# Optimization experiments

Measured on AMD Instinct MI355X. Metric: run time of the kernel, lower is better.

The kernel has to match this reference:

```python
import jax, jax.numpy as jnp
import numpy as np

D_MODEL = 1024
N_HEADS = 16
D_K = D_MODEL // N_HEADS
NEG = -1e9


def setup_inputs() -> dict:
    key = jax.random.key(0)
    ks = jax.random.split(key, 14)
    b, sq, sk = 4, 2048, 2048
    s = 1.0 / np.sqrt(D_MODEL)
    inp = {
        "Q": jax.random.normal(ks[0], (b, sq, D_MODEL), jnp.float32),
        "K": jax.random.normal(ks[1], (b, sk, D_MODEL), jnp.float32),
        "V": jax.random.normal(ks[2], (b, sk, D_MODEL), jnp.float32),
        "mask": jax.random.randint(ks[3], (b, sk), 0, 2, jnp.int32),
        "relative_logits": jax.random.normal(ks[4], (1, N_HEADS, sq, sk), jnp.float32),
        "Wq": jax.random.normal(ks[5], (D_MODEL, D_MODEL), jnp.float32) * s,
        "bq": jnp.zeros((D_MODEL,), jnp.float32),
        "Wk": jax.random.normal(ks[6], (D_MODEL, D_MODEL), jnp.float32) * s,
        "bk": jnp.zeros((D_MODEL,), jnp.float32),
        "Wv": jax.random.normal(ks[7], (D_MODEL, D_MODEL), jnp.float32) * s,
        "bv": jnp.zeros((D_MODEL,), jnp.float32),
        "Wo": jax.random.normal(ks[8], (D_MODEL, D_MODEL), jnp.float32) * s,
        "bo": jnp.zeros((D_MODEL,), jnp.float32),
    }
    return inp


def reference(Q, K, V, mask, relative_logits, Wq, bq, Wk, bk, Wv, bv, Wo, bo):
    b, sq, _ = Q.shape
    sk = K.shape[1]
    # projections -> [b, h, s, d_k]
    q = (Q @ Wq + bq).reshape(b, sq, N_HEADS, D_K).transpose(0, 2, 1, 3)
    k = (K @ Wk + bk).reshape(b, sk, N_HEADS, D_K).transpose(0, 2, 1, 3)
    v = (V @ Wv + bv).reshape(b, sk, N_HEADS, D_K).transpose(0, 2, 1, 3)
    scores = jnp.einsum("bhqd,bhkd->bhqk", q, k) / jnp.sqrt(jnp.float32(D_K))
    scores = scores + relative_logits
    # 2D mask [b, sk] -> [b, 1, 1, sk]; masked_fill where mask == 0
    m = mask[:, None, None, :]
    scores = jnp.where(m == 0, jnp.float32(NEG), scores)
    attn = jax.nn.softmax(scores, axis=-1)  # dropout = identity (eval mode)
    out = jnp.einsum("bhqk,bhkd->bhqd", attn, v)
    out = out.transpose(0, 2, 1, 3).reshape(b, sq, N_HEADS * D_K)
    out = out @ Wo + bo
    return (out, attn)
```

## Files before the change

### kernel.cpp

```cpp
#include <hip/hip_runtime.h>
#include <hip/hip_fp16.h>

typedef _Float16 f16;
typedef __attribute__((ext_vector_type(4))) _Float16 f16x4;
typedef __attribute__((ext_vector_type(8))) _Float16 f16x8;
typedef __attribute__((ext_vector_type(4))) float f32x4;

#define S_LEN 2048
#define D_MODEL 1024
#define N_HEADS 16
#define D_K 64
#define BATCH 4

#define EXP_NEG8 3.35462627903e-4f

#define LBAR() do { asm volatile("s_waitcnt lgkmcnt(0)" ::: "memory"); \
                    __builtin_amdgcn_s_barrier(); } while (0)

__global__ void cvt_f32_f16(const float* __restrict__ src, f16* __restrict__ dst, int n4) {
  int i = blockIdx.x * blockDim.x + threadIdx.x;
  if (i < n4) {
    const float4 v = reinterpret_cast<const float4*>(src)[i];
    f16x4 h;
    h.x = (f16)v.x; h.y = (f16)v.y; h.z = (f16)v.z; h.w = (f16)v.w;
    reinterpret_cast<f16x4*>(dst)[i] = h;
  }
}

__global__ void cvt3(const float* __restrict__ s0, const float* __restrict__ s1,
                     const float* __restrict__ s2, f16* __restrict__ d0, f16* __restrict__ d1,
                     f16* __restrict__ d2, int n4) {
  const float* s = blockIdx.y == 0 ? s0 : (blockIdx.y == 1 ? s1 : s2);
  f16* d = blockIdx.y == 0 ? d0 : (blockIdx.y == 1 ? d1 : d2);
  int i = blockIdx.x * blockDim.x + threadIdx.x;
  if (i < n4) {
    const float4 v = reinterpret_cast<const float4*>(s)[i];
    f16x4 h;
    h.x = (f16)v.x; h.y = (f16)v.y; h.z = (f16)v.z; h.w = (f16)v.w;
    reinterpret_cast<f16x4*>(d)[i] = h;
  }
}

__global__ void wtrans4(const float* __restrict__ W0, const float* __restrict__ W1,
                        const float* __restrict__ W2, const float* __restrict__ W3,
                        f16* __restrict__ T0, f16* __restrict__ T1, f16* __restrict__ T2,
                        f16* __restrict__ T3) {
  const float* W = blockIdx.z == 0 ? W0 : (blockIdx.z == 1 ? W1 : (blockIdx.z == 2 ? W2 : W3));
  f16* WT = blockIdx.z == 0 ? T0 : (blockIdx.z == 1 ? T1 : (blockIdx.z == 2 ? T2 : T3));
  __shared__ float tile[32][33];
  const int n0 = blockIdx.x * 32, k0 = blockIdx.y * 32;
  const int tx = threadIdx.x, ty = threadIdx.y;
#pragma unroll
  for (int i = 0; i < 4; ++i)
    tile[ty + i * 8][tx] = W[(size_t)(k0 + ty + i * 8) * D_MODEL + n0 + tx];
  __syncthreads();
#pragma unroll
  for (int i = 0; i < 4; ++i)
    WT[(size_t)(n0 + ty + i * 8) * D_MODEL + k0 + tx] = (f16)tile[tx][ty + i * 8];
}

__global__ __launch_bounds__(256, 3) void gemmQKV(const f16* __restrict__ Qh, const f16* __restrict__ Kh,
                                                  const f16* __restrict__ Vh, const f16* __restrict__ WqT,
                                                  const f16* __restrict__ WkT, const f16* __restrict__ WvT,
                                                  const float* __restrict__ bq, const float* __restrict__ bk,
                                                  const float* __restrict__ bv, f16* __restrict__ qb,
                                                  f16* __restrict__ kb, f16* __restrict__ vTb) {
  const int z = blockIdx.z;
  const f16* A = z == 0 ? Qh : (z == 1 ? Kh : Vh);
  const f16* BT = z == 0 ? WqT : (z == 1 ? WkT : WvT);
  const float* bias = z == 0 ? bq : (z == 1 ? bk : bv);

  __shared__ f16 As[2][128 * 40];
  __shared__ f16 Bs[2][128 * 40];
  const int t = threadIdx.x;
  const int lane = t & 63, wid = t >> 6;
  const int wm = wid >> 1, wn = wid & 1;
  const int lr = lane & 15, lg = lane >> 4;
  const int bm = blockIdx.y * 128, bn = blockIdx.x * 128;

  f32x4 acc[4][4] = {};

  const int r0s = t >> 2, g0 = (t & 3) * 8;
  const f16* gA0 = &A[(size_t)(bm + r0s) * 1024 + g0];
  const f16* gA1 = gA0 + (size_t)64 * 1024;
  const f16* gB0 = &BT[(size_t)(bn + r0s) * 1024 + g0];
  const f16* gB1 = gB0 + (size_t)64 * 1024;
  const int dst0 = r0s * 40 + g0, dst1 = (r0s + 64) * 40 + g0;

  int4 sA0, sA1, sB0, sB1;
  auto GLOAD = [&](int k0) {
    sA0 = *reinterpret_cast<const int4*>(gA0 + k0);
    sA1 = *reinterpret_cast<const int4*>(gA1 + k0);
    sB0 = *reinterpret_cast<const int4*>(gB0 + k0);
    sB1 = *reinterpret_cast<const int4*>(gB1 + k0);
  };
  auto DSW = [&](int bb) {
    *reinterpret_cast<int4*>(&As[bb][dst0]) = sA0;
    *reinterpret_cast<int4*>(&As[bb][dst1]) = sA1;
    *reinterpret_cast<int4*>(&Bs[bb][dst0]) = sB0;
    *reinterpret_cast<int4*>(&Bs[bb][dst1]) = sB1;
  };
  auto LDF = [&](int bb, int kk, f16x4 (&af)[4], f16x4 (&bf)[4]) {
#pragma unroll
    for (int mf = 0; mf < 4; ++mf)
      af[mf] = *reinterpret_cast<const f16x4*>(&As[bb][(wm * 64 + mf * 16 + lr) * 40 + kk * 16 + 4 * lg]);
#pragma unroll
    for (int nf = 0; nf < 4; ++nf)
      bf[nf] = *reinterpret_cast<const f16x4*>(&Bs[bb][(wn * 64 + nf * 16 + lr) * 40 + kk * 16 + 4 * lg]);
  };

  GLOAD(0);
  DSW(0);
  LBAR();
  if (z != 2) {
#pragma unroll 1
    for (int k = 0; k < 32; ++k) {
      if (k + 1 < 32) GLOAD((k + 1) * 32);
#pragma unroll
      for (int kk = 0; kk < 2; ++kk) {
        f16x4 af[4], bf[4];
        LDF(k & 1, kk, af, bf);
#pragma unroll
        for (int mf = 0; mf < 4; ++mf)
#pragma unroll
          for (int nf = 0; nf < 4; ++nf)
            acc[mf][nf] = __builtin_amdgcn_mfma_f32_16x16x16f16(af[mf], bf[nf], acc[mf][nf], 0, 0, 0);
      }
      if (k + 1 < 32) {
        DSW((k + 1) & 1);
        LBAR();
      }
    }
  } else {
#pragma unroll 1
    for (int k = 0; k < 32; ++k) {
      if (k + 1 < 32) GLOAD((k + 1) * 32);
#pragma unroll
      for (int kk = 0; kk < 2; ++kk) {
        f16x4 af[4], bf[4];
        LDF(k & 1, kk, af, bf);
#pragma unroll
        for (int mf = 0; mf < 4; ++mf)
#pragma unroll
          for (int nf = 0; nf < 4; ++nf)
            acc[mf][nf] = __builtin_amdgcn_mfma_f32_16x16x16f16(bf[nf], af[mf], acc[mf][nf], 0, 0, 0);
      }
      if (k + 1 < 32) {
        DSW((k + 1) & 1);
        LBAR();
      }
    }
  }

  if (z != 2) {
    const float scale = z == 0 ? 0.125f : 1.f;
    f16* outp = z == 0 ? qb : kb;
#pragma unroll
    for (int mf = 0; mf < 4; ++mf)
#pragma unroll
      for (int nf = 0; nf < 4; ++nf)
#pragma unroll
        for (int i = 0; i < 4; ++i) {
          const int mrow = bm + wm * 64 + mf * 16 + 4 * lg + i;
          const int ncol = bn + wn * 64 + nf * 16 + lr;
          const float v = (acc[mf][nf][i] + bias[ncol]) * scale;
          const int b = mrow >> 11, s = mrow & 2047;
          const int h = ncol >> 6, d = ncol & 63;
          outp[((size_t)(b * N_HEADS + h) * S_LEN + s) * D_K + d] = (f16)v;
        }
  } else {
#pragma unroll
    for (int mf = 0; mf < 4; ++mf)
#pragma unroll
      for (int nf = 0; nf < 4; ++nf)
#pragma unroll
        for (int i = 0; i < 4; ++i) {
          const int srow = bm + wm * 64 + mf * 16 + lr;
          const int dcol = bn + wn * 64 + nf * 16 + 4 * lg + i;
          const float v = acc[mf][nf][i] + bias[dcol];
          const int b = srow >> 11, s = srow & 2047;
          const int h = dcol >> 6, d = dcol & 63;
          vTb[((size_t)(b * N_HEADS + h) * D_K + d) * S_LEN + s] = (f16)v;
        }
  }
}

__global__ __launch_bounds__(256, 3) void gemmO(const f16* __restrict__ A, const f16* __restrict__ BT,
                                                const float* __restrict__ bias, float* __restrict__ outp) {
  __shared__ f16 As[2][128 * 40];
  __shared__ f16 Bs[2][128 * 40];
  const int t = threadIdx.x;
  const int lane = t & 63, wid = t >> 6;
  const int wm = wid >> 1, wn = wid & 1;
  const int lr = lane & 15, lg = lane >> 4;
  const int bm = blockIdx.y * 128, bn = blockIdx.x * 128;

  f32x4 acc[4][4] = {};

  const int r0s = t >> 2, g0 = (t & 3) * 8;
  const f16* gA0 = &A[(size_t)(bm + r0s) * 1024 + g0];
  const f16* gA1 = gA0 + (size_t)64 * 1024;
  const f16* gB0 = &BT[(size_t)(bn + r0s) * 1024 + g0];
  const f16* gB1 = gB0 + (size_t)64 * 1024;
  const int dst0 = r0s * 40 + g0, dst1 = (r0s + 64) * 40 + g0;

  int4 sA0, sA1, sB0, sB1;
  auto GLOAD = [&](int k0) {
    sA0 = *reinterpret_cast<const int4*>(gA0 + k0);
    sA1 = *reinterpret_cast<const int4*>(gA1 + k0);
    sB0 = *reinterpret_cast<const int4*>(gB0 + k0);
    sB1 = *reinterpret_cast<const int4*>(gB1 + k0);
  };
  auto DSW = [&](int bb) {
    *reinterpret_cast<int4*>(&As[bb][dst0]) = sA0;
    *reinterpret_cast<int4*>(&As[bb][dst1]) = sA1;
    *reinterpret_cast<int4*>(&Bs[bb][dst0]) = sB0;
    *reinterpret_cast<int4*>(&Bs[bb][dst1]) = sB1;
  };

  GLOAD(0);
  DSW(0);
  LBAR();
#pragma unroll 1
  for (int k = 0; k < 32; ++k) {
    if (k + 1 < 32) GLOAD((k + 1) * 32);
#pragma unroll
    for (int kk = 0; kk < 2; ++kk) {
      f16x4 af[4], bf[4];
#pragma unroll
      for (int mf = 0; mf < 4; ++mf)
        af[mf] = *reinterpret_cast<const f16x4*>(&As[k & 1][(wm * 64 + mf * 16 + lr) * 40 + kk * 16 + 4 * lg]);
#pragma unroll
      for (int nf = 0; nf < 4; ++nf)
        bf[nf] = *reinterpret_cast<const f16x4*>(&Bs[k & 1][(wn * 64 + nf * 16 + lr) * 40 + kk * 16 + 4 * lg]);
#pragma unroll
      for (int mf = 0; mf < 4; ++mf)
#pragma unroll
        for (int nf = 0; nf < 4; ++nf)
          acc[mf][nf] = __builtin_amdgcn_mfma_f32_16x16x16f16(af[mf], bf[nf], acc[mf][nf], 0, 0, 0);
    }
    if (k + 1 < 32) {
      DSW((k + 1) & 1);
      LBAR();
    }
  }

#pragma unroll
  for (int mf = 0; mf < 4; ++mf)
#pragma unroll
    for (int nf = 0; nf < 4; ++nf)
#pragma unroll
      for (int i = 0; i < 4; ++i) {
        const int mrow = bm + wm * 64 + mf * 16 + 4 * lg + i;
        const int ncol = bn + wn * 64 + nf * 16 + lr;
        outp[(size_t)mrow * D_MODEL + ncol] = acc[mf][nf][i] + bias[ncol];
      }
}

__global__ __launch_bounds__(256, 3) void attn_fused2(const f16* __restrict__ qg, const f16* __restrict__ kg,
                                                      const f16* __restrict__ vTg, const f16* __restrict__ rel16,
                                                      const int* __restrict__ mask, float* __restrict__ attn_out,
                                                      f16* __restrict__ ctx) {
  const int b = blockIdx.x & 3, qt = blockIdx.x >> 2;
  const int h = blockIdx.y;
  const int t = threadIdx.x, w = t >> 6, lane = t & 63;
  const int lr = lane & 15, lg = lane >> 4;
  const int lr7 = lr & 7;
  const int Ld8 = lane >> 3, Lm8 = lane & 7;

  __shared__ f16 Kc[2][64 * 64];
  __shared__ f16 Vc[2][64 * 64];
  __shared__ f16 Rc[2][64 * 64];
  __shared__ f16 maskh[S_LEN];

  for (int i = t; i < S_LEN; i += 256) maskh[i] = mask[b * S_LEN + i] ? (f16)EXP_NEG8 : (f16)0.f;

  const size_t bh = (size_t)(b * N_HEADS + h);
  const f16* qbh = qg + bh * S_LEN * D_K;
  const f16* kbh = kg + bh * S_LEN * D_K;
  const f16* vbh = vTg + bh * (size_t)D_K * S_LEN;
  const f16* relh = rel16 + (size_t)h * S_LEN * S_LEN;

  const int r0 = qt * 64 + w * 16;
  const int myq = r0 + lr;
  float* attnq = attn_out + bh * (size_t)S_LEN * S_LEN + (size_t)myq * S_LEN;

  const int row0 = w * 16 + Ld8;
  const int row1 = row0 + 8;
  const f16* gK0 = kbh + (size_t)row0 * D_K + Lm8 * 8;
  const f16* gK1 = kbh + (size_t)row1 * D_K + Lm8 * 8;
  const f16* gV0 = vbh + (size_t)row0 * S_LEN + Lm8 * 8;
  const f16* gV1 = vbh + (size_t)row1 * S_LEN + Lm8 * 8;
  const f16* gR0 = relh + (size_t)(qt * 64 + row0) * S_LEN + Lm8 * 8;
  const f16* gR1 = relh + (size_t)(qt * 64 + row1) * S_LEN + Lm8 * 8;
  const int dK0 = row0 * 64 + ((Lm8 ^ Ld8) << 3);
  const int dK1 = row1 * 64 + ((Lm8 ^ Ld8) << 3);
  const int dVR0 = row0 * 64 + ((((Lm8 << 1) ^ (Ld8 << 1)) & 15) << 2);
  const int dVR1 = row1 * 64 + ((((Lm8 << 1) ^ (Ld8 << 1)) & 15) << 2);

  f16x8 qf8[2];
#pragma unroll
  for (int p = 0; p < 2; ++p)
    qf8[p] = *reinterpret_cast<const f16x8*>(&qbh[(size_t)myq * D_K + 32 * p + 8 * lg]);

  int4 sK0, sK1, sV0, sV1, sR0, sR1;
  auto GK = [&](int c0) {
    sK0 = *reinterpret_cast<const int4*>(gK0 + (size_t)c0 * D_K);
    sK1 = *reinterpret_cast<const int4*>(gK1 + (size_t)c0 * D_K);
  };
  auto GV = [&](int c0) {
    sV0 = *reinterpret_cast<const int4*>(gV0 + c0);
    sV1 = *reinterpret_cast<const int4*>(gV1 + c0);
  };
  auto GR = [&](int c0) {
    sR0 = *reinterpret_cast<const int4*>(gR0 + c0);
    sR1 = *reinterpret_cast<const int4*>(gR1 + c0);
  };
  auto DSW1 = [&](int bb) {
    *reinterpret_cast<int4*>(&Kc[bb][dK0]) = sK0;
    *reinterpret_cast<int4*>(&Kc[bb][dK1]) = sK1;
    *reinterpret_cast<int4*>(&Rc[bb][dVR0]) = sR0;
    *reinterpret_cast<int4*>(&Rc[bb][dVR1]) = sR1;
  };
  auto DSW2 = [&](int bb) {
    *reinterpret_cast<int4*>(&Kc[bb][dK0]) = sK0;
    *reinterpret_cast<int4*>(&Kc[bb][dK1]) = sK1;
    *reinterpret_cast<int4*>(&Vc[bb][dVR0]) = sV0;
    *reinterpret_cast<int4*>(&Vc[bb][dVR1]) = sV1;
    *reinterpret_cast<int4*>(&Rc[bb][dVR0]) = sR0;
    *reinterpret_cast<int4*>(&Rc[bb][dVR1]) = sR1;
  };

  auto SCORES = [&](int bb, f32x4 (&sc)[4]) {
#pragma unroll
    for (int p = 0; p < 2; ++p) {
      const f16x4 qlo = __builtin_shufflevector(qf8[p], qf8[p], 0, 1, 2, 3);
      const f16x4 qhi = __builtin_shufflevector(qf8[p], qf8[p], 4, 5, 6, 7);
#pragma unroll
      for (int j = 0; j < 4; ++j) {
        const f16x8 kv = *reinterpret_cast<const f16x8*>(
            &Kc[bb][(16 * j + lr) * 64 + (((4 * p + lg) ^ lr7) << 3)]);
        sc[j] = __builtin_amdgcn_mfma_f32_16x16x16f16(
            __builtin_shufflevector(kv, kv, 0, 1, 2, 3), qlo, sc[j], 0, 0, 0);
        sc[j] = __builtin_amdgcn_mfma_f32_16x16x16f16(
            __builtin_shufflevector(kv, kv, 4, 5, 6, 7), qhi, sc[j], 0, 0, 0);
      }
    }
  };

  float sum = 0.f;
  GK(0);
  GR(0);
  DSW1(0);
  LBAR();
#pragma unroll 1
  for (int c = 0; c < 32; ++c) {
    if (c + 1 < 32) {
      GK((c + 1) * 64);
      GR((c + 1) * 64);
    }
    const int bb = c & 1;
    f32x4 sc[4] = {};
    SCORES(bb, sc);
#pragma unroll
    for (int j = 0; j < 4; ++j) {
      const int sgp = ((4 * j + lg) ^ (lr7 << 1)) & 15;
      const f16x4 rl = *reinterpret_cast<const f16x4*>(&Rc[bb][(w * 16 + lr) * 64 + (sgp << 2)]);
      const int col = c * 64 + 16 * j + 4 * lg;
      const f16x4 mh = *reinterpret_cast<const f16x4*>(&maskh[col]);
      sum += __expf(sc[j][0] + (float)rl[0]) * (float)mh[0] +
             __expf(sc[j][1] + (float)rl[1]) * (float)mh[1] +
             __expf(sc[j][2] + (float)rl[2]) * (float)mh[2] +
             __expf(sc[j][3] + (float)rl[3]) * (float)mh[3];
    }
    if (c + 1 < 32) {
      DSW1((c + 1) & 1);
      LBAR();
    }
  }
  sum += __shfl_xor(sum, 16, 64);
  sum += __shfl_xor(sum, 32, 64);
  const float inv = 1.f / sum;

  f32x4 pv[4] = {};
  GK(0);
  GV(0);
  GR(0);
  DSW2(0);
  LBAR();
#pragma unroll 1
  for (int c = 0; c < 32; ++c) {
    if (c + 1 < 32) {
      GK((c + 1) * 64);
      GV((c + 1) * 64);
      GR((c + 1) * 64);
    }
    const int bb = c & 1;
    f32x4 sc[4] = {};
    SCORES(bb, sc);
#pragma unroll
    for (int j = 0; j < 4; ++j) {
      const int sgp = ((4 * j + lg) ^ (lr7 << 1)) & 15;
      const f16x4 rl = *reinterpret_cast<const f16x4*>(&Rc[bb][(w * 16 + lr) * 64 + (sgp << 2)]);
      const int col = c * 64 + 16 * j + 4 * lg;
      const f16x4 mh = *reinterpret_cast<const f16x4*>(&maskh[col]);
      const float a0 = __expf(sc[j][0] + (float)rl[0]) * (float)mh[0] * inv;
      const float a1 = __expf(sc[j][1] + (float)rl[1]) * (float)mh[1] * inv;
      const float a2 = __expf(sc[j][2] + (float)rl[2]) * (float)mh[2] * inv;
      const float a3 = __expf(sc[j][3] + (float)rl[3]) * (float)mh[3] * inv;
      f32x4 av = {a0, a1, a2, a3};
      __builtin_nontemporal_store(av, reinterpret_cast<f32x4*>(&attnq[col]));
      f16x4 pf;
      pf.x = (f16)a0; pf.y = (f16)a1; pf.z = (f16)a2; pf.w = (f16)a3;
#pragma unroll
      for (int nf = 0; nf < 4; ++nf) {
        const f16x4 vf = *reinterpret_cast<const f16x4*>(&Vc[bb][(nf * 16 + lr) * 64 + (sgp << 2)]);
        pv[nf] = __builtin_amdgcn_mfma_f32_16x16x16f16(pf, vf, pv[nf], 0, 0, 0);
      }
    }
    if (c + 1 < 32) {
      DSW2((c + 1) & 1);
      LBAR();
    }
  }

#pragma unroll
  for (int nf = 0; nf < 4; ++nf)
#pragma unroll
    for (int i = 0; i < 4; ++i)
      ctx[(size_t)(b * S_LEN + r0 + 4 * lg + i) * D_MODEL + h * D_K + nf * 16 + lr] =
          (f16)pv[nf][i];
}

__global__ __launch_bounds__(256) void attn_single(const f16* __restrict__ qg, const f16* __restrict__ kg,
                                                   const f16* __restrict__ vTg, const float* __restrict__ relp,
                                                   const int* __restrict__ mask, float* __restrict__ attn_out,
                                                   f16* __restrict__ ctx) {
  const int b = blockIdx.x & 3, qt = blockIdx.x >> 2;
  const int h = blockIdx.y;
  const int t = threadIdx.x, w = t >> 6, lane = t & 63;
  const int lr = lane & 15, lg = lane >> 4;
  __shared__ float mask_f[S_LEN];

  for (int i = t; i < S_LEN; i += 256) mask_f[i] = mask[b * S_LEN + i] ? EXP_NEG8 : 0.f;
  __syncthreads();

  const size_t bh = (size_t)(b * N_HEADS + h);
  const f16* qbh = qg + bh * S_LEN * D_K;
  const f16* kbh = kg + bh * S_LEN * D_K;
  const f16* vbh = vTg + bh * (size_t)D_K * S_LEN;

  const int r0 = qt * 64 + w * 16;
  const int myq = r0 + lr;

  const float* relq32 = relp + (size_t)h * S_LEN * S_LEN + (size_t)myq * S_LEN;
  float* attnq = attn_out + bh * (size_t)S_LEN * S_LEN + (size_t)myq * S_LEN;

  f16x8 qf8[2];
#pragma unroll
  for (int p = 0; p < 2; ++p)
    qf8[p] = *reinterpret_cast<const f16x8*>(&qbh[(size_t)myq * D_K + 32 * p + 8 * lg]);

  float sum = 0.f;
  f32x4 pv[4] = {};

  auto CH = [&](int c0) {
    f32x4 sc[4] = {};
#pragma unroll
    for (int p = 0; p < 2; ++p) {
      const f16x4 qlo = __builtin_shufflevector(qf8[p], qf8[p], 0, 1, 2, 3);
      const f16x4 qhi = __builtin_shufflevector(qf8[p], qf8[p], 4, 5, 6, 7);
#pragma unroll
      for (int j = 0; j < 4; ++j) {
        const f16x8 kv = *reinterpret_cast<const f16x8*>(
            &kbh[(size_t)(c0 + 16 * j + lr) * D_K + 32 * p + 8 * lg]);
        sc[j] = __builtin_amdgcn_mfma_f32_16x16x16f16(
            __builtin_shufflevector(kv, kv, 0, 1, 2, 3), qlo, sc[j], 0, 0, 0);
        sc[j] = __builtin_amdgcn_mfma_f32_16x16x16f16(
            __builtin_shufflevector(kv, kv, 4, 5, 6, 7), qhi, sc[j], 0, 0, 0);
      }
    }
#pragma unroll
    for (int j = 0; j < 4; ++j) {
      const int col = c0 + 16 * j + 4 * lg;
      const float4 rl = *reinterpret_cast<const float4*>(&relq32[col]);
      const float4 mk = *reinterpret_cast<const float4*>(&mask_f[col]);
      const float a0 = __expf(sc[j][0] + rl.x) * mk.x;
      const float a1 = __expf(sc[j][1] + rl.y) * mk.y;
      const float a2 = __expf(sc[j][2] + rl.z) * mk.z;
      const float a3 = __expf(sc[j][3] + rl.w) * mk.w;
      sum += a0 + a1 + a2 + a3;
      f16x4 pf;
      pf.x = (f16)a0; pf.y = (f16)a1; pf.z = (f16)a2; pf.w = (f16)a3;
      *reinterpret_cast<float4*>(&attnq[col]) = make_float4(a0, a1, a2, a3);
#pragma unroll
      for (int nf = 0; nf < 4; ++nf) {
        const f16x4 vf = *reinterpret_cast<const f16x4*>(&vbh[(size_t)(nf * 16 + lr) * S_LEN + col]);
        pv[nf] = __builtin_amdgcn_mfma_f32_16x16x16f16(pf, vf, pv[nf], 0, 0, 0);
      }
    }
  };

#pragma unroll 1
  for (int c0 = 0; c0 < S_LEN; c0 += 64) CH(c0);

  sum += __shfl_xor(sum, 16, 64);
  sum += __shfl_xor(sum, 32, 64);
  const float inv = 1.f / sum;

  float ivr[4];
#pragma unroll
  for (int i = 0; i < 4; ++i) ivr[i] = __shfl(inv, 4 * lg + i, 64);
#pragma unroll
  for (int nf = 0; nf < 4; ++nf)
#pragma unroll
    for (int i = 0; i < 4; ++i)
      ctx[(size_t)(b * S_LEN + r0 + 4 * lg + i) * D_MODEL + h * D_K + nf * 16 + lr] =
          (f16)(pv[nf][i] * ivr[i]);

  float4* aw4 = reinterpret_cast<float4*>(attn_out + bh * (size_t)S_LEN * S_LEN + (size_t)r0 * S_LEN);
#pragma unroll 1
  for (int it = 0; it < 128; it += 4) {
#pragma unroll
    for (int u = 0; u < 4; ++u) {
      const float iv = __shfl(inv, (it + u) >> 3, 64);
      float4 v = aw4[(it + u) * 64 + lane];
      v.x *= iv; v.y *= iv; v.z *= iv; v.w *= iv;
      aw4[(it + u) * 64 + lane] = v;
    }
  }
}

extern "C" void kernel_launch(void* const* d_in, const int* in_sizes, int n_in,
                              void* d_out, int out_size, void* d_ws, size_t ws_size,
                              hipStream_t stream) {
  const float* Q    = (const float*)d_in[0];
  const float* K    = (const float*)d_in[1];
  const float* V    = (const float*)d_in[2];
  const int*   mask = (const int*)d_in[3];
  const float* rel  = (const float*)d_in[4];
  const float* Wq   = (const float*)d_in[5];
  const float* bq   = (const float*)d_in[6];
  const float* Wk   = (const float*)d_in[7];
  const float* bk   = (const float*)d_in[8];
  const float* Wv   = (const float*)d_in[9];
  const float* bv   = (const float*)d_in[10];
  const float* Wo   = (const float*)d_in[11];
  const float* bo   = (const float*)d_in[12];

  char* wsb = (char*)d_ws;
  const size_t XSZ = (size_t)BATCH * S_LEN * D_MODEL * sizeof(f16);
  const size_t WSZ = (size_t)D_MODEL * D_MODEL * sizeof(f16);
  f16* Qh  = (f16*)(wsb);
  f16* Kh  = (f16*)(wsb + XSZ);
  f16* Vh  = (f16*)(wsb + 2 * XSZ);
  f16* WqT = (f16*)(wsb + 3 * XSZ);
  f16* WkT = (f16*)(wsb + 3 * XSZ + WSZ);
  f16* WvT = (f16*)(wsb + 3 * XSZ + 2 * WSZ);
  f16* WoT = (f16*)(wsb + 3 * XSZ + 3 * WSZ);
  f16* qb  = (f16*)(wsb + 3 * XSZ + 4 * WSZ);
  f16* kb  = (f16*)(wsb + 4 * XSZ + 4 * WSZ);
  f16* vTb = (f16*)(wsb + 5 * XSZ + 4 * WSZ);
  f16* ctx = (f16*)(wsb + 6 * XSZ + 4 * WSZ);

  const size_t BASE  = 7 * XSZ + 4 * WSZ;
  const size_t RELSZ = (size_t)N_HEADS * S_LEN * S_LEN * sizeof(f16);
  f16* rel16 = (f16*)(wsb + BASE);
  const bool r16 = ws_size >= BASE + RELSZ;

  float* out0 = (float*)d_out;
  float* attn = out0 + (size_t)BATCH * S_LEN * D_MODEL;

  const int n4 = BATCH * S_LEN * D_MODEL / 4;
  cvt3<<<dim3(n4 / 256, 3), 256, 0, stream>>>(Q, K, V, Qh, Kh, Vh, n4);
  wtrans4<<<dim3(32, 32, 4), dim3(32, 8), 0, stream>>>(Wq, Wk, Wv, Wo, WqT, WkT, WvT, WoT);
  if (r16) {
    const int nr4 = N_HEADS * S_LEN * S_LEN / 4;
    cvt_f32_f16<<<dim3(nr4 / 256), 256, 0, stream>>>(rel, rel16, nr4);
  }

  gemmQKV<<<dim3(8, 64, 3), 256, 0, stream>>>(Qh, Kh, Vh, WqT, WkT, WvT, bq, bk, bv, qb, kb, vTb);

  if (r16) {
    attn_fused2<<<dim3(BATCH * (S_LEN / 64), N_HEADS), 256, 0, stream>>>(qb, kb, vTb, rel16, mask,
                                                                         attn, ctx);
  } else {
    attn_single<<<dim3(BATCH * (S_LEN / 64), N_HEADS), 256, 0, stream>>>(qb, kb, vTb, rel, mask,
                                                                         attn, ctx);
  }

  gemmO<<<dim3(8, 64), 256, 0, stream>>>(ctx, WoT, bo, out0);
}
```

Measured before the change: 694.1 us.

## Process two 64-row query tiles per block in fused attention kernel

Result: faster. 674.0 us (median of 2 runs) (-2.9%).

```diff
diff --git a/kernel.cpp b/kernel.cpp
--- a/kernel.cpp
+++ b/kernel.cpp
@@ -257,7 +257,7 @@
       }
 }
 
-__global__ __launch_bounds__(256, 3) void attn_fused2(const f16* __restrict__ qg, const f16* __restrict__ kg,
+__global__ __launch_bounds__(256, 2) void attn_fused2(const f16* __restrict__ qg, const f16* __restrict__ kg,
                                                       const f16* __restrict__ vTg, const f16* __restrict__ rel16,
                                                       const int* __restrict__ mask, float* __restrict__ attn_out,
                                                       f16* __restrict__ ctx) {
@@ -270,7 +270,7 @@
 
   __shared__ f16 Kc[2][64 * 64];
   __shared__ f16 Vc[2][64 * 64];
-  __shared__ f16 Rc[2][64 * 64];
+  __shared__ f16 Rc[2][128 * 64];
   __shared__ f16 maskh[S_LEN];
 
   for (int i = t; i < S_LEN; i += 256) maskh[i] = mask[b * S_LEN + i] ? (f16)EXP_NEG8 : (f16)0.f;
@@ -281,9 +281,10 @@
   const f16* vbh = vTg + bh * (size_t)D_K * S_LEN;
   const f16* relh = rel16 + (size_t)h * S_LEN * S_LEN;
 
-  const int r0 = qt * 64 + w * 16;
+  const int r0 = qt * 128 + w * 16;
   const int myq = r0 + lr;
-  float* attnq = attn_out + bh * (size_t)S_LEN * S_LEN + (size_t)myq * S_LEN;
+  float* attnq0 = attn_out + bh * (size_t)S_LEN * S_LEN + (size_t)myq * S_LEN;
+  float* attnq1 = attnq0 + (size_t)64 * S_LEN;
 
   const int row0 = w * 16 + Ld8;
   const int row1 = row0 + 8;
@@ -291,19 +292,25 @@
   const f16* gK1 = kbh + (size_t)row1 * D_K + Lm8 * 8;
   const f16* gV0 = vbh + (size_t)row0 * S_LEN + Lm8 * 8;
   const f16* gV1 = vbh + (size_t)row1 * S_LEN + Lm8 * 8;
-  const f16* gR0 = relh + (size_t)(qt * 64 + row0) * S_LEN + Lm8 * 8;
-  const f16* gR1 = relh + (size_t)(qt * 64 + row1) * S_LEN + Lm8 * 8;
+  const f16* gR0 = relh + (size_t)(qt * 128 + row0) * S_LEN + Lm8 * 8;
+  const f16* gR1 = relh + (size_t)(qt * 128 + row1) * S_LEN + Lm8 * 8;
+  const f16* gR2 = gR0 + (size_t)64 * S_LEN;
+  const f16* gR3 = gR1 + (size_t)64 * S_LEN;
   const int dK0 = row0 * 64 + ((Lm8 ^ Ld8) << 3);
   const int dK1 = row1 * 64 + ((Lm8 ^ Ld8) << 3);
   const int dVR0 = row0 * 64 + ((((Lm8 << 1) ^ (Ld8 << 1)) & 15) << 2);
   const int dVR1 = row1 * 64 + ((((Lm8 << 1) ^ (Ld8 << 1)) & 15) << 2);
-
-  f16x8 qf8[2];
-#pragma unroll
-  for (int p = 0; p < 2; ++p)
-    qf8[p] = *reinterpret_cast<const f16x8*>(&qbh[(size_t)myq * D_K + 32 * p + 8 * lg]);
-
-  int4 sK0, sK1, sV0, sV1, sR0, sR1;
+  const int dVR2 = dVR0 + 64 * 64;
+  const int dVR3 = dVR1 + 64 * 64;
+
+  f16x8 qf80[2], qf81[2];
+#pragma unroll
+  for (int p = 0; p < 2; ++p) {
+    qf80[p] = *reinterpret_cast<const f16x8*>(&qbh[(size_t)myq * D_K + 32 * p + 8 * lg]);
+    qf81[p] = *reinterpret_cast<const f16x8*>(&qbh[(size_t)(myq + 64) * D_K + 32 * p + 8 * lg]);
+  }
+
+  int4 sK0, sK1, sV0, sV1, sR0, sR1, sR2, sR3;
   auto GK = [&](int c0) {
     sK0 = *reinterpret_cast<const int4*>(gK0 + (size_t)c0 * D_K);
     sK1 = *reinterpret_cast<const int4*>(gK1 + (size_t)c0 * D_K);
@@ -315,12 +322,16 @@
   auto GR = [&](int c0) {
     sR0 = *reinterpret_cast<const int4*>(gR0 + c0);
     sR1 = *reinterpret_cast<const int4*>(gR1 + c0);
+    sR2 = *reinterpret_cast<const int4*>(gR2 + c0);
+    sR3 = *reinterpret_cast<const int4*>(gR3 + c0);
   };
   auto DSW1 = [&](int bb) {
     *reinterpret_cast<int4*>(&Kc[bb][dK0]) = sK0;
     *reinterpret_cast<int4*>(&Kc[bb][dK1]) = sK1;
     *reinterpret_cast<int4*>(&Rc[bb][dVR0]) = sR0;
     *reinterpret_cast<int4*>(&Rc[bb][dVR1]) = sR1;
+    *reinterpret_cast<int4*>(&Rc[bb][dVR2]) = sR2;
+    *reinterpret_cast<int4*>(&Rc[bb][dVR3]) = sR3;
   };
   auto DSW2 = [&](int bb) {
     *reinterpret_cast<int4*>(&Kc[bb][dK0]) = sK0;
@@ -329,9 +340,11 @@
     *reinterpret_cast<int4*>(&Vc[bb][dVR1]) = sV1;
     *reinterpret_cast<int4*>(&Rc[bb][dVR0]) = sR0;
     *reinterpret_cast<int4*>(&Rc[bb][dVR1]) = sR1;
-  };
-
-  auto SCORES = [&](int bb, f32x4 (&sc)[4]) {
+    *reinterpret_cast<int4*>(&Rc[bb][dVR2]) = sR2;
+    *reinterpret_cast<int4*>(&Rc[bb][dVR3]) = sR3;
+  };
+
+  auto SCORES = [&](int bb, const f16x8 (&qf8)[2], f32x4 (&sc)[4]) {
 #pragma unroll
     for (int p = 0; p < 2; ++p) {
       const f16x4 qlo = __builtin_shufflevector(qf8[p], qf8[p], 0, 1, 2, 3);
@@ -348,7 +361,7 @@
     }
   };
 
-  float sum = 0.f;
+  float sum0 = 0.f, sum1 = 0.f;
   GK(0);
   GR(0);
   DSW1(0);
@@ -360,29 +373,38 @@
       GR((c + 1) * 64);
     }
     const int bb = c & 1;
-    f32x4 sc[4] = {};
-    SCORES(bb, sc);
+    f32x4 sc0[4] = {}, sc1[4] = {};
+    SCORES(bb, qf80, sc0);
+    SCORES(bb, qf81, sc1);
 #pragma unroll
     for (int j = 0; j < 4; ++j) {
       const int sgp = ((4 * j + lg) ^ (lr7 << 1)) & 15;
-      const f16x4 rl = *reinterpret_cast<const f16x4*>(&Rc[bb][(w * 16 + lr) * 64 + (sgp << 2)]);
       const int col = c * 64 + 16 * j + 4 * lg;
       const f16x4 mh = *reinterpret_cast<const f16x4*>(&maskh[col]);
-      sum += __expf(sc[j][0] + (float)rl[0]) * (float)mh[0] +
-             __expf(sc[j][1] + (float)rl[1]) * (float)mh[1] +
-             __expf(sc[j][2] + (float)rl[2]) * (float)mh[2] +
-             __expf(sc[j][3] + (float)rl[3]) * (float)mh[3];
+      const f16x4 rl0 = *reinterpret_cast<const f16x4*>(&Rc[bb][(w * 16 + lr) * 64 + (sgp << 2)]);
+      const f16x4 rl1 = *reinterpret_cast<const f16x4*>(&Rc[bb][(w * 16 + lr + 64) * 64 + (sgp << 2)]);
+      sum0 += __expf(sc0[j][0] + (float)rl0[0]) * (float)mh[0] +
+              __expf(sc0[j][1] + (float)rl0[1]) * (float)mh[1] +
+              __expf(sc0[j][2] + (float)rl0[2]) * (float)mh[2] +
+              __expf(sc0[j][3] + (float)rl0[3]) * (float)mh[3];
+      sum1 += __expf(sc1[j][0] + (float)rl1[0]) * (float)mh[0] +
+              __expf(sc1[j][1] + (float)rl1[1]) * (float)mh[1] +
+              __expf(sc1[j][2] + (float)rl1[2]) * (float)mh[2] +
+              __expf(sc1[j][3] + (float)rl1[3]) * (float)mh[3];
     }
     if (c + 1 < 32) {
       DSW1((c + 1) & 1);
       LBAR();
     }
   }
-  sum += __shfl_xor(sum, 16, 64);
-  sum += __shfl_xor(sum, 32, 64);
-  const float inv = 1.f / sum;
-
-  f32x4 pv[4] = {};
+  sum0 += __shfl_xor(sum0, 16, 64);
+  sum0 += __shfl_xor(sum0, 32, 64);
+  sum1 += __shfl_xor(sum1, 16, 64);
+  sum1 += __shfl_xor(sum1, 32, 64);
+  const float inv0 = 1.f / sum0;
+  const float inv1 = 1.f / sum1;
+
+  f32x4 pv0[4] = {}, pv1[4] = {};
   GK(0);
   GV(0);
   GR(0);
@@ -396,26 +418,36 @@
       GR((c + 1) * 64);
     }
     const int bb = c & 1;
-    f32x4 sc[4] = {};
-    SCORES(bb, sc);
+    f32x4 sc0[4] = {}, sc1[4] = {};
+    SCORES(bb, qf80, sc0);
+    SCORES(bb, qf81, sc1);
 #pragma unroll
     for (int j = 0; j < 4; ++j) {
       const int sgp = ((4 * j + lg) ^ (lr7 << 1)) & 15;
-      const f16x4 rl = *reinterpret_cast<const f16x4*>(&Rc[bb][(w * 16 + lr) * 64 + (sgp << 2)]);
       const int col = c * 64 + 16 * j + 4 * lg;
       const f16x4 mh = *reinterpret_cast<const f16x4*>(&maskh[col]);
-      const float a0 = __expf(sc[j][0] + (float)rl[0]) * (float)mh[0] * inv;
-      const float a1 = __expf(sc[j][1] + (float)rl[1]) * (float)mh[1] * inv;
-      const float a2 = __expf(sc[j][2] + (float)rl[2]) * (float)mh[2] * inv;
-      const float a3 = __expf(sc[j][3] + (float)rl[3]) * (float)mh[3] * inv;
-      f32x4 av = {a0, a1, a2, a3};
-      __builtin_nontemporal_store(av, reinterpret_cast<f32x4*>(&attnq[col]));
-      f16x4 pf;
-      pf.x = (f16)a0; pf.y = (f16)a1; pf.z = (f16)a2; pf.w = (f16)a3;
+      const f16x4 rl0 = *reinterpret_cast<const f16x4*>(&Rc[bb][(w * 16 + lr) * 64 + (sgp << 2)]);
+      const f16x4 rl1 = *reinterpret_cast<const f16x4*>(&Rc[bb][(w * 16 + lr + 64) * 64 + (sgp << 2)]);
+      const float a00 = __expf(sc0[j][0] + (float)rl0[0]) * (float)mh[0] * inv0;
+      const float a01 = __expf(sc0[j][1] + (float)rl0[1]) * (float)mh[1] * inv0;
+      const float a02 = __expf(sc0[j][2] + (float)rl0[2]) * (float)mh[2] * inv0;
+      const float a03 = __expf(sc0[j][3] + (float)rl0[3]) * (float)mh[3] * inv0;
+      const float a10 = __expf(sc1[j][0] + (float)rl1[0]) * (float)mh[0] * inv1;
+      const float a11 = __expf(sc1[j][1] + (float)rl1[1]) * (float)mh[1] * inv1;
+      const float a12 = __expf(sc1[j][2] + (float)rl1[2]) * (float)mh[2] * inv1;
+      const float a13 = __expf(sc1[j][3] + (float)rl1[3]) * (float)mh[3] * inv1;
+      f32x4 av0 = {a00, a01, a02, a03};
+      f32x4 av1 = {a10, a11, a12, a13};
+      __builtin_nontemporal_store(av0, reinterpret_cast<f32x4*>(&attnq0[col]));
+      __builtin_nontemporal_store(av1, reinterpret_cast<f32x4*>(&attnq1[col]));
+      f16x4 pf0, pf1;
+      pf0.x = (f16)a00; pf0.y = (f16)a01; pf0.z = (f16)a02; pf0.w = (f16)a03;
+      pf1.x = (f16)a10; pf1.y = (f16)a11; pf1.z = (f16)a12; pf1.w = (f16)a13;
 #pragma unroll
       for (int nf = 0; nf < 4; ++nf) {
         const f16x4 vf = *reinterpret_cast<const f16x4*>(&Vc[bb][(nf * 16 + lr) * 64 + (sgp << 2)]);
-        pv[nf] = __builtin_amdgcn_mfma_f32_16x16x16f16(pf, vf, pv[nf], 0, 0, 0);
+        pv0[nf] = __builtin_amdgcn_mfma_f32_16x16x16f16(pf0, vf, pv0[nf], 0, 0, 0);
+        pv1[nf] = __builtin_amdgcn_mfma_f32_16x16x16f16(pf1, vf, pv1[nf], 0, 0, 0);
       }
     }
     if (c + 1 < 32) {
@@ -427,9 +459,12 @@
 #pragma unroll
   for (int nf = 0; nf < 4; ++nf)
 #pragma unroll
-    for (int i = 0; i < 4; ++i)
+    for (int i = 0; i < 4; ++i) {
       ctx[(size_t)(b * S_LEN + r0 + 4 * lg + i) * D_MODEL + h * D_K + nf * 16 + lr] =
-          (f16)pv[nf][i];
+          (f16)pv0[nf][i];
+      ctx[(size_t)(b * S_LEN + r0 + 64 + 4 * lg + i) * D_MODEL + h * D_K + nf * 16 + lr] =
+          (f16)pv1[nf][i];
+    }
 }
 
 __global__ __launch_bounds__(256) void attn_single(const f16* __restrict__ qg, const f16* __restrict__ kg,
@@ -582,8 +617,8 @@
   gemmQKV<<<dim3(8, 64, 3), 256, 0, stream>>>(Qh, Kh, Vh, WqT, WkT, WvT, bq, bk, bv, qb, kb, vTb);
 
   if (r16) {
-    attn_fused2<<<dim3(BATCH * (S_LEN / 64), N_HEADS), 256, 0, stream>>>(qb, kb, vTb, rel16, mask,
-                                                                         attn, ctx);
+    attn_fused2<<<dim3(BATCH * (S_LEN / 128), N_HEADS), 256, 0, stream>>>(qb, kb, vTb, rel16, mask,
+                                                                          attn, ctx);
   } else {
     attn_single<<<dim3(BATCH * (S_LEN / 64), N_HEADS), 256, 0, stream>>>(qb, kb, vTb, rel, mask,
                                                                          attn, ctx);
```
